# Optimization experiments

Hardware: AMD Instinct MI355X
Metric: run time of the kernel (lower is better)

## Reference

```python
import jax, jax.numpy as jnp
import numpy as np

N_RAYS, N_SAMPLES, HIDDEN, N_VOXELS = 8192, 256, 64, 1000


def setup_inputs() -> dict:
    key = jax.random.key(0)
    ks = jax.random.split(key, 10)
    ray_start = jax.random.normal(ks[0], (N_RAYS, 3), jnp.float32)
    ray_dir = jax.random.normal(ks[1], (N_RAYS, 3), jnp.float32)
    ray_dir = ray_dir / jnp.linalg.norm(ray_dir, axis=-1, keepdims=True)
    # monotonically increasing depths along each ray
    sampled_depth = jnp.sort(jax.random.uniform(ks[2], (N_RAYS, N_SAMPLES), jnp.float32) * 4.0 + 0.5, axis=-1)
    sampled_dists = jax.random.uniform(ks[3], (N_RAYS, N_SAMPLES), jnp.float32) * 0.02 + 1e-3
    sampled_idx = jax.random.randint(ks[4], (N_RAYS, N_SAMPLES), -333, N_VOXELS).astype(jnp.int64)
    W1 = jax.random.normal(ks[5], (3, HIDDEN), jnp.float32) * 0.5
    b1 = jnp.zeros((HIDDEN,), jnp.float32)
    w_sigma = jax.random.normal(ks[6], (HIDDEN,), jnp.float32) * 0.5
    W_rgb = jax.random.normal(ks[7], (HIDDEN, 3), jnp.float32) * 0.5
    W_dir = jax.random.normal(ks[8], (3, 3), jnp.float32) * 0.5
    b_rgb = jnp.zeros((3,), jnp.float32)
    return {"ray_start": ray_start, "ray_dir": ray_dir, "sampled_depth": sampled_depth,
            "sampled_dists": sampled_dists, "sampled_idx": sampled_idx,
            "W1": W1, "b1": b1, "w_sigma": w_sigma, "W_rgb": W_rgb, "W_dir": W_dir, "b_rgb": b_rgb}


def _volume_render(ray_start, ray_dir, sampled_depth, sampled_dists, sampled_idx,
                   W1, b1, w_sigma, W_rgb, W_dir, b_rgb):
    # sampled_xyz = ray(ray_start, ray_dir, depth)
    xyz = ray_start[:, None, :] + ray_dir[:, None, :] * sampled_depth[..., None]  # [N,P,3]
    h = jax.nn.relu(jnp.einsum('npi,ih->nph', xyz, W1) + b1)                      # [N,P,H]
    sigma = jnp.einsum('nph,h->np', h, w_sigma)                                   # [N,P]
    rgb = jax.nn.sigmoid(jnp.einsum('nph,hc->npc', h, W_rgb)
                         + jnp.einsum('ni,ic->nc', ray_dir, W_dir)[:, None, :] + b_rgb)  # [N,P,3]
    mask = (sampled_idx != -1).astype(sigma.dtype)                                # [N,P]
    # free_energy = relu(sigma) * dists * 7.0, scattered back with zeros at misses
    free_energy = jax.nn.relu(sigma) * sampled_dists * 7.0 * mask
    shifted = jnp.concatenate([jnp.zeros_like(free_energy[:, :1]), free_energy[:, :-1]], axis=-1)
    a = 1.0 - jnp.exp(-free_energy)
    b = jnp.exp(-jnp.cumsum(shifted, axis=-1))
    probs = a * b                                                                 # [N,P]
    depths = jnp.sum(sampled_depth * probs, axis=-1)                              # [N]
    missed = 1.0 - jnp.sum(probs, axis=-1)                                        # [N]
    colors = jnp.sum(rgb * probs[..., None], axis=-2)                             # [N,3]
    return jnp.concatenate([colors, depths[:, None], missed[:, None], probs], axis=-1)  # [N, 3+1+1+P]


def reference(ray_start, ray_dir, sampled_depth, sampled_dists, sampled_idx,
              W1, b1, w_sigma, W_rgb, W_dir, b_rgb):
    return _volume_render(ray_start, ray_dir, sampled_depth, sampled_dists, sampled_idx,
                          W1, b1, w_sigma, W_rgb, W_dir, b_rgb)
```

## Files before the change

kernel.cpp:

```cpp
#include <hip/hip_runtime.h>

#define NRAYS 8192
#define NS    256
#define HID   64
#define NPAIR 32
#define RPB   8
#define SPT   8

typedef _Float16 f16x2 __attribute__((ext_vector_type(2)));

static __device__ __forceinline__ float fdot2(f16x2 a, f16x2 b, float c) {
    return __builtin_amdgcn_fdot2(a, b, c, false);
}
static __device__ __forceinline__ f16x2 mk2(float a, float b) {
    f16x2 v; v.x = (_Float16)a; v.y = (_Float16)b; return v;
}

struct __align__(16) W4  { f16x2 ws, wr, wg, wb; };
struct __align__(8)  AB2 { f16x2 A, B; };

__global__ __launch_bounds__(256) void vr_kernel(
    const float* __restrict__ ray_start,
    const float* __restrict__ ray_dir,
    const float* __restrict__ sampled_depth,
    const float* __restrict__ sampled_dists,
    const int*   __restrict__ sampled_idx,
    const float* __restrict__ W1,
    const float* __restrict__ b1,
    const float* __restrict__ w_sigma,
    const float* __restrict__ W_rgb,
    const float* __restrict__ W_dir,
    const float* __restrict__ b_rgb,
    float* __restrict__ out)
{
    __shared__ W4  sW[NPAIR];
    __shared__ AB2 sAB[RPB][NPAIR];

    const int t = threadIdx.x;
    if (t < NPAIR) {
        const int h0 = 2*t, h1 = 2*t + 1;
        W4 w;
        w.ws = mk2(w_sigma[h0],    w_sigma[h1]);
        w.wr = mk2(W_rgb[h0*3+0],  W_rgb[h1*3+0]);
        w.wg = mk2(W_rgb[h0*3+1],  W_rgb[h1*3+1]);
        w.wb = mk2(W_rgb[h0*3+2],  W_rgb[h1*3+2]);
        sW[t] = w;
    }
    {
        const int rr  = t >> 5;
        const int k   = t & (NPAIR - 1);
        const int ray = blockIdx.x * RPB + rr;
        const float ox = ray_start[ray*3+0], oy = ray_start[ray*3+1], oz = ray_start[ray*3+2];
        const float dx = ray_dir[ray*3+0],  dy = ray_dir[ray*3+1],  dz = ray_dir[ray*3+2];
        const int h0 = 2*k, h1 = 2*k + 1;
        const float u0 = W1[h0], u1 = W1[HID + h0], u2 = W1[2*HID + h0];
        const float v0 = W1[h1], v1 = W1[HID + h1], v2 = W1[2*HID + h1];
        const float A0 = fmaf(u0, ox, fmaf(u1, oy, fmaf(u2, oz, b1[h0])));
        const float B0 = fmaf(u0, dx, fmaf(u1, dy, u2 * dz));
        const float A1 = fmaf(v0, ox, fmaf(v1, oy, fmaf(v2, oz, b1[h1])));
        const float B1 = fmaf(v0, dx, fmaf(v1, dy, v2 * dz));
        AB2 e; e.A = mk2(A0, A1); e.B = mk2(B0, B1);
        sAB[rr][k] = e;
    }
    __syncthreads();

    const int lane = t & 63;
    const int wave = t >> 6;
    const int hl   = lane & 31;
    const int r    = wave * 2 + (lane >> 5);
    const int ray  = blockIdx.x * RPB + r;

    const float dx = ray_dir[ray*3+0], dy = ray_dir[ray*3+1], dz = ray_dir[ray*3+2];
    const float dwr = fmaf(dx, W_dir[0], fmaf(dy, W_dir[3], fmaf(dz, W_dir[6], b_rgb[0])));
    const float dwg = fmaf(dx, W_dir[1], fmaf(dy, W_dir[4], fmaf(dz, W_dir[7], b_rgb[1])));
    const float dwb = fmaf(dx, W_dir[2], fmaf(dy, W_dir[5], fmaf(dz, W_dir[8], b_rgb[2])));

    const size_t rbase = (size_t)ray * NS + (size_t)hl * SPT;
    const float4 dep0 = ((const float4*)(sampled_depth + rbase))[0];
    const float4 dep1 = ((const float4*)(sampled_depth + rbase))[1];
    const float4 dst0 = ((const float4*)(sampled_dists + rbase))[0];
    const float4 dst1 = ((const float4*)(sampled_dists + rbase))[1];
    const int4   vi0  = ((const int4*)(sampled_idx + rbase))[0];
    const int4   vi1  = ((const int4*)(sampled_idx + rbase))[1];

    const float dpt[SPT] = {dep0.x, dep0.y, dep0.z, dep0.w, dep1.x, dep1.y, dep1.z, dep1.w};
    const float dsv[SPT] = {dst0.x, dst0.y, dst0.z, dst0.w, dst1.x, dst1.y, dst1.z, dst1.w};
    const int   vid[SPT] = {vi0.x, vi0.y, vi0.z, vi0.w, vi1.x, vi1.y, vi1.z, vi1.w};

    f16x2 d2[SPT];
#pragma unroll
    for (int j = 0; j < SPT; ++j) d2[j] = mk2(dpt[j], dpt[j]);
    const f16x2 zero2 = mk2(0.f, 0.f);

    float sig[SPT] = {0,0,0,0,0,0,0,0};
    float cr[SPT]  = {0,0,0,0,0,0,0,0};
    float cg[SPT]  = {0,0,0,0,0,0,0,0};
    float cb[SPT]  = {0,0,0,0,0,0,0,0};

#pragma unroll 4
    for (int k = 0; k < NPAIR; ++k) {
        const W4  w  = sW[k];
        const AB2 ab = sAB[r][k];
#pragma unroll
        for (int j = 0; j < SPT; ++j) {
            f16x2 hv = __builtin_elementwise_fma(ab.B, d2[j], ab.A);
            hv = __builtin_elementwise_max(hv, zero2);
            sig[j] = fdot2(hv, w.ws, sig[j]);
            cr[j]  = fdot2(hv, w.wr, cr[j]);
            cg[j]  = fdot2(hv, w.wg, cg[j]);
            cb[j]  = fdot2(hv, w.wb, cb[j]);
        }
    }

    float c[SPT];
    float run = 0.f;
#pragma unroll
    for (int j = 0; j < SPT; ++j) {
        float f = fmaxf(sig[j], 0.f) * dsv[j] * 7.0f;
        if (vid[j] == -1) f = 0.f;
        run += f;
        c[j] = run;
    }

    float tot = run;
#pragma unroll
    for (int off = 1; off < 32; off <<= 1) {
        const float v = __shfl_up(tot, off, 32);
        if (hl >= off) tot += v;
    }
    const float base = tot - run;

    float Eprev = __expf(-base);
    float prob[SPT];
    float s0 = 0.f, s1 = 0.f, s2 = 0.f, s3 = 0.f, s4 = 0.f;
#pragma unroll
    for (int j = 0; j < SPT; ++j) {
        const float Ej = __expf(-(base + c[j]));
        const float p  = Eprev - Ej;
        Eprev = Ej;
        prob[j] = p;
        const float rr = __builtin_amdgcn_rcpf(1.f + __expf(-(cr[j] + dwr)));
        const float gg = __builtin_amdgcn_rcpf(1.f + __expf(-(cg[j] + dwg)));
        const float bb = __builtin_amdgcn_rcpf(1.f + __expf(-(cb[j] + dwb)));
        s0 += p;
        s1 = fmaf(dpt[j], p, s1);
        s2 = fmaf(rr, p, s2);
        s3 = fmaf(gg, p, s3);
        s4 = fmaf(bb, p, s4);
    }

#pragma unroll
    for (int off = 16; off >= 1; off >>= 1) {
        s0 += __shfl_xor(s0, off, 32);
        s1 += __shfl_xor(s1, off, 32);
        s2 += __shfl_xor(s2, off, 32);
        s3 += __shfl_xor(s3, off, 32);
        s4 += __shfl_xor(s4, off, 32);
    }

    float* orow = out + (size_t)ray * (NS + 5);
#pragma unroll
    for (int j = 0; j < SPT; ++j)
        orow[5 + SPT*hl + j] = prob[j];

    if (hl == 0) {
        orow[0] = s2;
        orow[1] = s3;
        orow[2] = s4;
        orow[3] = s1;
        orow[4] = 1.f - s0;
    }
}

extern "C" void kernel_launch(void* const* d_in, const int* in_sizes, int n_in,
                              void* d_out, int out_size, void* d_ws, size_t ws_size,
                              hipStream_t stream)
{
    vr_kernel<<<NRAYS / RPB, 256, 0, stream>>>(
        (const float*)d_in[0],
        (const float*)d_in[1],
        (const float*)d_in[2],
        (const float*)d_in[3],
        (const int*)  d_in[4],
        (const float*)d_in[5],
        (const float*)d_in[6],
        (const float*)d_in[7],
        (const float*)d_in[8],
        (const float*)d_in[9],
        (const float*)d_in[10],
        (float*)d_out);
}
```

Before: 104.2 us.

## Compute hidden-layer output projections with MFMA matrix instructions instead of fdot2

Replaces the per-sample fdot2 loops over hidden units with 16x16x32 f16 MFMA instructions. Each wave builds the ReLU hidden activations as A fragments, and the sigma/rgb weights are padded into a 16-column B operand. Results are staged through per-wave LDS and then redistributed so that one full wave handles each ray's 256 samples for the scan and compositing, looping over two rays per wave. This cuts VALU work in the main loop. In exchange it wastes 12 of 16 MFMA output columns, adds LDS round trips, and drops the block barrier, relying on each wave reading only the shared data it wrote itself.

After: 102.7 us. About the same (-1.5%).

```diff
diff --git a/kernel.cpp b/kernel.cpp
--- a/kernel.cpp
+++ b/kernel.cpp
@@ -5,21 +5,19 @@
 #define HID   64
 #define NPAIR 32
 #define RPB   8
-#define SPT   8
 
 typedef _Float16 f16x2 __attribute__((ext_vector_type(2)));
-
-static __device__ __forceinline__ float fdot2(f16x2 a, f16x2 b, float c) {
-    return __builtin_amdgcn_fdot2(a, b, c, false);
-}
+typedef _Float16 f16x8 __attribute__((ext_vector_type(8)));
+typedef float    f32x4 __attribute__((ext_vector_type(4)));
+
 static __device__ __forceinline__ f16x2 mk2(float a, float b) {
     f16x2 v; v.x = (_Float16)a; v.y = (_Float16)b; return v;
 }
 
-struct __align__(16) W4  { f16x2 ws, wr, wg, wb; };
-struct __align__(8)  AB2 { f16x2 A, B; };
-
-__global__ __launch_bounds__(256) void vr_kernel(
+struct __align__(8) AB2 { f16x2 A, B; };
+union AFrag { f16x8 v; f16x2 h[4]; };
+
+__global__ __launch_bounds__(256, 4) void vr_kernel(
     const float* __restrict__ ray_start,
     const float* __restrict__ ray_dir,
     const float* __restrict__ sampled_depth,
@@ -33,19 +31,12 @@
     const float* __restrict__ b_rgb,
     float* __restrict__ out)
 {
-    __shared__ W4  sW[NPAIR];
-    __shared__ AB2 sAB[RPB][NPAIR];
+    __shared__ AB2   sAB[RPB][NPAIR];
+    __shared__ f16x2 sDep[RPB][NS];
+    __shared__ __align__(16) float sOut[4][4][264];
 
     const int t = threadIdx.x;
-    if (t < NPAIR) {
-        const int h0 = 2*t, h1 = 2*t + 1;
-        W4 w;
-        w.ws = mk2(w_sigma[h0],    w_sigma[h1]);
-        w.wr = mk2(W_rgb[h0*3+0],  W_rgb[h1*3+0]);
-        w.wg = mk2(W_rgb[h0*3+1],  W_rgb[h1*3+1]);
-        w.wb = mk2(W_rgb[h0*3+2],  W_rgb[h1*3+2]);
-        sW[t] = w;
-    }
+
     {
         const int rr  = t >> 5;
         const int k   = t & (NPAIR - 1);
@@ -62,113 +53,157 @@
         AB2 e; e.A = mk2(A0, A1); e.B = mk2(B0, B1);
         sAB[rr][k] = e;
     }
-    __syncthreads();
+    {
+        const int rr  = t >> 5;
+        const int i   = t & 31;
+        const int ray = blockIdx.x * RPB + rr;
+        const size_t base = (size_t)ray * NS + (size_t)i * 8;
+        const float4 d0 = ((const float4*)(sampled_depth + base))[0];
+        const float4 d1 = ((const float4*)(sampled_depth + base))[1];
+        f16x2* dst = &sDep[rr][i*8];
+        dst[0] = mk2(d0.x, d0.x); dst[1] = mk2(d0.y, d0.y);
+        dst[2] = mk2(d0.z, d0.z); dst[3] = mk2(d0.w, d0.w);
+        dst[4] = mk2(d1.x, d1.x); dst[5] = mk2(d1.y, d1.y);
+        dst[6] = mk2(d1.z, d1.z); dst[7] = mk2(d1.w, d1.w);
+    }
 
     const int lane = t & 63;
     const int wave = t >> 6;
-    const int hl   = lane & 31;
-    const int r    = wave * 2 + (lane >> 5);
-    const int ray  = blockIdx.x * RPB + r;
-
-    const float dx = ray_dir[ray*3+0], dy = ray_dir[ray*3+1], dz = ray_dir[ray*3+2];
-    const float dwr = fmaf(dx, W_dir[0], fmaf(dy, W_dir[3], fmaf(dz, W_dir[6], b_rgb[0])));
-    const float dwg = fmaf(dx, W_dir[1], fmaf(dy, W_dir[4], fmaf(dz, W_dir[7], b_rgb[1])));
-    const float dwb = fmaf(dx, W_dir[2], fmaf(dy, W_dir[5], fmaf(dz, W_dir[8], b_rgb[2])));
-
-    const size_t rbase = (size_t)ray * NS + (size_t)hl * SPT;
-    const float4 dep0 = ((const float4*)(sampled_depth + rbase))[0];
-    const float4 dep1 = ((const float4*)(sampled_depth + rbase))[1];
-    const float4 dst0 = ((const float4*)(sampled_dists + rbase))[0];
-    const float4 dst1 = ((const float4*)(sampled_dists + rbase))[1];
-    const int4   vi0  = ((const int4*)(sampled_idx + rbase))[0];
-    const int4   vi1  = ((const int4*)(sampled_idx + rbase))[1];
-
-    const float dpt[SPT] = {dep0.x, dep0.y, dep0.z, dep0.w, dep1.x, dep1.y, dep1.z, dep1.w};
-    const float dsv[SPT] = {dst0.x, dst0.y, dst0.z, dst0.w, dst1.x, dst1.y, dst1.z, dst1.w};
-    const int   vid[SPT] = {vi0.x, vi0.y, vi0.z, vi0.w, vi1.x, vi1.y, vi1.z, vi1.w};
-
-    f16x2 d2[SPT];
-#pragma unroll
-    for (int j = 0; j < SPT; ++j) d2[j] = mk2(dpt[j], dpt[j]);
+    const int col  = lane & 15;
+    const int g    = lane >> 4;
+
+    f16x8 bf0, bf1;
+#pragma unroll
+    for (int e = 0; e < 8; ++e) {
+        const int u0 = g*8 + e, u1 = 32 + g*8 + e;
+        float v0 = 0.f, v1 = 0.f;
+        if (col == 0)     { v0 = w_sigma[u0];           v1 = w_sigma[u1]; }
+        else if (col < 4) { v0 = W_rgb[u0*3 + (col-1)]; v1 = W_rgb[u1*3 + (col-1)]; }
+        bf0[e] = (_Float16)v0; bf1[e] = (_Float16)v1;
+    }
+
     const f16x2 zero2 = mk2(0.f, 0.f);
-
-    float sig[SPT] = {0,0,0,0,0,0,0,0};
-    float cr[SPT]  = {0,0,0,0,0,0,0,0};
-    float cg[SPT]  = {0,0,0,0,0,0,0,0};
-    float cb[SPT]  = {0,0,0,0,0,0,0,0};
-
-#pragma unroll 4
-    for (int k = 0; k < NPAIR; ++k) {
-        const W4  w  = sW[k];
-        const AB2 ab = sAB[r][k];
-#pragma unroll
-        for (int j = 0; j < SPT; ++j) {
-            f16x2 hv = __builtin_elementwise_fma(ab.B, d2[j], ab.A);
-            hv = __builtin_elementwise_max(hv, zero2);
-            sig[j] = fdot2(hv, w.ws, sig[j]);
-            cr[j]  = fdot2(hv, w.wr, cr[j]);
-            cg[j]  = fdot2(hv, w.wg, cg[j]);
-            cb[j]  = fdot2(hv, w.wb, cb[j]);
-        }
-    }
-
-    float c[SPT];
-    float run = 0.f;
-#pragma unroll
-    for (int j = 0; j < SPT; ++j) {
-        float f = fmaxf(sig[j], 0.f) * dsv[j] * 7.0f;
-        if (vid[j] == -1) f = 0.f;
-        run += f;
-        c[j] = run;
-    }
-
-    float tot = run;
-#pragma unroll
-    for (int off = 1; off < 32; off <<= 1) {
-        const float v = __shfl_up(tot, off, 32);
-        if (hl >= off) tot += v;
-    }
-    const float base = tot - run;
-
-    float Eprev = __expf(-base);
-    float prob[SPT];
-    float s0 = 0.f, s1 = 0.f, s2 = 0.f, s3 = 0.f, s4 = 0.f;
-#pragma unroll
-    for (int j = 0; j < SPT; ++j) {
-        const float Ej = __expf(-(base + c[j]));
-        const float p  = Eprev - Ej;
-        Eprev = Ej;
-        prob[j] = p;
-        const float rr = __builtin_amdgcn_rcpf(1.f + __expf(-(cr[j] + dwr)));
-        const float gg = __builtin_amdgcn_rcpf(1.f + __expf(-(cg[j] + dwg)));
-        const float bb = __builtin_amdgcn_rcpf(1.f + __expf(-(cb[j] + dwb)));
-        s0 += p;
-        s1 = fmaf(dpt[j], p, s1);
-        s2 = fmaf(rr, p, s2);
-        s3 = fmaf(gg, p, s3);
-        s4 = fmaf(bb, p, s4);
-    }
-
-#pragma unroll
-    for (int off = 16; off >= 1; off >>= 1) {
-        s0 += __shfl_xor(s0, off, 32);
-        s1 += __shfl_xor(s1, off, 32);
-        s2 += __shfl_xor(s2, off, 32);
-        s3 += __shfl_xor(s3, off, 32);
-        s4 += __shfl_xor(s4, off, 32);
-    }
-
-    float* orow = out + (size_t)ray * (NS + 5);
-#pragma unroll
-    for (int j = 0; j < SPT; ++j)
-        orow[5 + SPT*hl + j] = prob[j];
-
-    if (hl == 0) {
-        orow[0] = s2;
-        orow[1] = s3;
-        orow[2] = s4;
-        orow[3] = s1;
-        orow[4] = 1.f - s0;
+    const f32x4 zacc  = {0.f, 0.f, 0.f, 0.f};
+
+#pragma unroll 1
+    for (int q = 0; q < 2; ++q) {
+        const int r   = wave*2 + q;
+        const int ray = blockIdx.x * RPB + r;
+
+        AB2 c0[4], c1[4];
+#pragma unroll
+        for (int d = 0; d < 4; ++d) {
+            c0[d] = sAB[r][4*g + d];
+            c1[d] = sAB[r][16 + 4*g + d];
+        }
+
+        f32x4 acc[16];
+#pragma unroll
+        for (int b = 0; b < 16; ++b) acc[b] = zacc;
+
+#pragma unroll
+        for (int b = 0; b < 16; ++b) {
+            const f16x2 t2 = sDep[r][16*b + col];
+            AFrag a0, a1;
+#pragma unroll
+            for (int d = 0; d < 4; ++d) {
+                a0.h[d] = __builtin_elementwise_max(
+                    __builtin_elementwise_fma(c0[d].B, t2, c0[d].A), zero2);
+                a1.h[d] = __builtin_elementwise_max(
+                    __builtin_elementwise_fma(c1[d].B, t2, c1[d].A), zero2);
+            }
+            acc[b] = __builtin_amdgcn_mfma_f32_16x16x32_f16(a0.v, bf0, acc[b], 0, 0, 0);
+            acc[b] = __builtin_amdgcn_mfma_f32_16x16x32_f16(a1.v, bf1, acc[b], 0, 0, 0);
+        }
+
+        if (col < 4) {
+#pragma unroll
+            for (int b = 0; b < 16; ++b) {
+                float4 v; v.x = acc[b][0]; v.y = acc[b][1]; v.z = acc[b][2]; v.w = acc[b][3];
+                *(float4*)&sOut[wave][col][16*b + 4*g] = v;
+            }
+        }
+
+        const int sb = 4*lane;
+        const float4 sg  = *(const float4*)&sOut[wave][0][sb];
+        const float4 cr4 = *(const float4*)&sOut[wave][1][sb];
+        const float4 cg4 = *(const float4*)&sOut[wave][2][sb];
+        const float4 cb4 = *(const float4*)&sOut[wave][3][sb];
+
+        const size_t rb = (size_t)ray * NS + (size_t)sb;
+        const float4 dpt = *(const float4*)(sampled_depth + rb);
+        const float4 dsv = *(const float4*)(sampled_dists + rb);
+        const int4   vid = *(const int4*)(sampled_idx + rb);
+
+        const float ddx = ray_dir[ray*3+0], ddy = ray_dir[ray*3+1], ddz = ray_dir[ray*3+2];
+        const float dwr = fmaf(ddx, W_dir[0], fmaf(ddy, W_dir[3], fmaf(ddz, W_dir[6], b_rgb[0])));
+        const float dwg = fmaf(ddx, W_dir[1], fmaf(ddy, W_dir[4], fmaf(ddz, W_dir[7], b_rgb[1])));
+        const float dwb = fmaf(ddx, W_dir[2], fmaf(ddy, W_dir[5], fmaf(ddz, W_dir[8], b_rgb[2])));
+
+        const float sigA[4] = {sg.x,  sg.y,  sg.z,  sg.w};
+        const float crA[4]  = {cr4.x, cr4.y, cr4.z, cr4.w};
+        const float cgA[4]  = {cg4.x, cg4.y, cg4.z, cg4.w};
+        const float cbA[4]  = {cb4.x, cb4.y, cb4.z, cb4.w};
+        const float dptA[4] = {dpt.x, dpt.y, dpt.z, dpt.w};
+        const float dsvA[4] = {dsv.x, dsv.y, dsv.z, dsv.w};
+        const int   vidA[4] = {vid.x, vid.y, vid.z, vid.w};
+
+        float c[4]; float run = 0.f;
+#pragma unroll
+        for (int j = 0; j < 4; ++j) {
+            float f = fmaxf(sigA[j], 0.f) * dsvA[j] * 7.0f;
+            if (vidA[j] == -1) f = 0.f;
+            run += f; c[j] = run;
+        }
+
+        float tot = run;
+#pragma unroll
+        for (int off = 1; off < 64; off <<= 1) {
+            const float v = __shfl_up(tot, off, 64);
+            if (lane >= off) tot += v;
+        }
+        const float base = tot - run;
+
+        float Eprev = __expf(-base);
+        float prob[4];
+        float sS = 0.f, sD = 0.f, sR = 0.f, sG = 0.f, sB = 0.f;
+#pragma unroll
+        for (int j = 0; j < 4; ++j) {
+            const float Ej = __expf(-(base + c[j]));
+            const float p  = Eprev - Ej;
+            Eprev = Ej;
+            prob[j] = p;
+            const float rr2 = __builtin_amdgcn_rcpf(1.f + __expf(-(crA[j] + dwr)));
+            const float gg2 = __builtin_amdgcn_rcpf(1.f + __expf(-(cgA[j] + dwg)));
+            const float bb2 = __builtin_amdgcn_rcpf(1.f + __expf(-(cbA[j] + dwb)));
+            sS += p;
+            sD = fmaf(dptA[j], p, sD);
+            sR = fmaf(rr2, p, sR);
+            sG = fmaf(gg2, p, sG);
+            sB = fmaf(bb2, p, sB);
+        }
+
+#pragma unroll
+        for (int off = 32; off >= 1; off >>= 1) {
+            sS += __shfl_xor(sS, off);
+            sD += __shfl_xor(sD, off);
+            sR += __shfl_xor(sR, off);
+            sG += __shfl_xor(sG, off);
+            sB += __shfl_xor(sB, off);
+        }
+
+        float* orow = out + (size_t)ray * (NS + 5);
+#pragma unroll
+        for (int j = 0; j < 4; ++j)
+            orow[5 + sb + j] = prob[j];
+
+        if (lane == 0) {
+            orow[0] = sR;
+            orow[1] = sG;
+            orow[2] = sB;
+            orow[3] = sD;
+            orow[4] = 1.f - sS;
+        }
     }
 }
 
```
